# Kernel optimization log

Measured on AMD Instinct MI355X. Metric: run time of the kernel, lower is better.

## Reference

```python
import jax, jax.numpy as jnp
import numpy as np

B, S, D = 2, 2048, 768
H, STRIDE = 12, 8
HD = D // H  # 64


def setup_inputs() -> dict:
    key = jax.random.key(0)
    k0, k1, k2 = jax.random.split(key, 3)
    x = jax.random.normal(k0, (B, S, D), dtype=jnp.float32)
    qkv_w = jax.random.normal(k1, (3 * D, D), dtype=jnp.float32) * 0.02
    qkv_b = jnp.zeros((3 * D,), dtype=jnp.float32)
    out_w = jax.random.normal(k2, (D, D), dtype=jnp.float32) * 0.02
    out_b = jnp.zeros((D,), dtype=jnp.float32)
    return {"x": x, "qkv_w": qkv_w, "qkv_b": qkv_b, "out_w": out_w, "out_b": out_b}


def _stride_mask(S, stride, causal):
    i = jnp.arange(S)[:, None]
    j = jnp.arange(S)[None, :]
    strided = (j % stride == 0)
    if causal:
        strided = strided & (j <= i)
    # diagonal always attended; previous token attended for i > 0
    return strided | (j == i) | (j == i - 1)


def reference(x, qkv_w, qkv_b, out_w, out_b):
    Bx, Sx, Dx = x.shape
    qkv = x @ qkv_w.T + qkv_b                      # [B,S,3D]
    qkv = qkv.reshape(Bx, Sx, 3, H, HD)
    q, k, v = jnp.transpose(qkv, (2, 0, 3, 1, 4))  # each [B,H,S,HD]
    scale = HD ** -0.5
    attn = jnp.einsum('bhid,bhjd->bhij', q, k) * scale  # [B,H,S,S]
    mask = _stride_mask(Sx, STRIDE, True)          # [S,S] bool
    attn = jnp.where(mask[None, None], attn, -jnp.inf)
    a = jax.nn.softmax(attn, axis=-1)
    # every row has at least the diagonal unmasked, so no NaN rows;
    # nan_to_num kept for exact parity with the torch module
    a = jnp.nan_to_num(a, nan=0.0)
    out = jnp.einsum('bhij,bhjd->bhid', a, v)      # [B,H,S,HD]
    out = jnp.transpose(out, (0, 2, 1, 3)).reshape(Bx, Sx, Dx)
    return out @ out_w.T + out_b
```

## Files before the change

kernel.cpp:

```cpp
#include <hip/hip_runtime.h>
#include <hip/hip_bf16.h>
#include <stdint.h>

#define H_   12
#define S_   2048
#define D_   768
#define HD_  64
#define MS_  256

typedef __bf16 bf16_8 __attribute__((ext_vector_type(8)));
typedef float  f32_4  __attribute__((ext_vector_type(4)));

typedef __attribute__((address_space(1))) void* gas_ptr;
typedef __attribute__((address_space(3))) void* las_ptr;

__device__ __forceinline__ void g2l16(const void* g, void* l) {
  __builtin_amdgcn_global_load_lds((gas_ptr)g, (las_ptr)l, 16, 0, 0);
}

__device__ __forceinline__ f32_4 mfma16(bf16_8 a, bf16_8 b, f32_4 c) {
  return __builtin_amdgcn_mfma_f32_16x16x32_bf16(a, b, c, 0, 0, 0);
}

__device__ __forceinline__ bf16_8 ld8(const __hip_bfloat16* p) {
  return *reinterpret_cast<const bf16_8*>(p);
}

__global__ __launch_bounds__(256) void cvt3_f32_bf16(
    const float* __restrict__ a, const float* __restrict__ b,
    const float* __restrict__ c, __hip_bfloat16* __restrict__ out,
    int na4, int nb4) {
  const int t = blockIdx.x * 256 + threadIdx.x;
  float4 f;
  if (t < na4)            f = reinterpret_cast<const float4*>(a)[t];
  else if (t < na4 + nb4) f = reinterpret_cast<const float4*>(b)[t - na4];
  else                    f = reinterpret_cast<const float4*>(c)[t - na4 - nb4];
  union { __hip_bfloat16 h[4]; ushort4 u; } p;
  p.h[0] = __float2bfloat16(f.x);
  p.h[1] = __float2bfloat16(f.y);
  p.h[2] = __float2bfloat16(f.z);
  p.h[3] = __float2bfloat16(f.w);
  reinterpret_cast<ushort4*>(out)[t] = p.u;
}

template <int MODE, int BN>
__global__ __launch_bounds__(256, 4) void gemm_bt(
    const __hip_bfloat16* __restrict__ A, const __hip_bfloat16* __restrict__ B,
    const float* __restrict__ bias,
    __hip_bfloat16* __restrict__ O0, __hip_bfloat16* __restrict__ O1,
    __hip_bfloat16* __restrict__ O2, __hip_bfloat16* __restrict__ O3,
    __hip_bfloat16* __restrict__ O4, float* __restrict__ OF,
    int M, int N, int K) {
  constexpr int NTJ  = BN / 32;
  constexpr int HB   = BN * 32;
  constexpr int DB   = (MODE == 1) ? 2 : 1;
  constexpr int ABUF = 64 * 64;
  constexpr int BBUF = BN * 64;
  __shared__ __bf16 sA[DB * ABUF];
  __shared__ __bf16 sB[DB * BBUF];
  const int tid  = threadIdx.x;
  const int lane = tid & 63;
  const int wv   = tid >> 6;

  const int nwg  = gridDim.x * gridDim.y;
  const int hw   = blockIdx.y * gridDim.x + blockIdx.x;
  const int swz  = (hw & 7) * (nwg >> 3) + (hw >> 3);
  const int bx   = swz % gridDim.x;
  const int by   = swz / gridDim.x;

  const int m0 = by * 64;
  const int n0 = bx * BN;
  const int wr = (wv >> 1) * 32;
  const int wc = (wv & 1) * (BN / 2);

  f32_4 acc[2][NTJ] = {};

  const __hip_bfloat16* aS = A + (size_t)(m0 + (tid >> 2)) * K + ((tid & 3) << 3);
  const __hip_bfloat16* bS = B + (size_t)(n0 + (tid >> 2)) * K + ((tid & 3) << 3);
  const size_t half = (size_t)64 * K;
  __bf16* dA = &sA[tid * 8];
  __bf16* dB = &sB[tid * 8];

  const int fr = lane & 15;
  const int kq = (lane >> 4) << 3;

  auto stage = [&](int k0, int buf) {
    const __hip_bfloat16* a = aS + k0;
    const __hip_bfloat16* b = bS + k0;
    __bf16* da = dA + buf * ABUF;
    __bf16* db = dB + buf * BBUF;
    g2l16(a,      da);
    g2l16(a + 32, da + 2048);
    g2l16(b,      db);
    if constexpr (BN == 128) {
      g2l16(b + half,      db + 2048);
      g2l16(b + 32,        db + 4096);
      g2l16(b + half + 32, db + 4096 + 2048);
    } else {
      g2l16(b + 32, db + 2048);
    }
  };

  auto compute = [&](const __bf16* bA, const __bf16* bB) {
#pragma unroll
    for (int kk = 0; kk < 2; ++kk) {
      bf16_8 af[2], bfm[NTJ];
#pragma unroll
      for (int t = 0; t < 2; ++t)
        af[t] = *reinterpret_cast<const bf16_8*>(
            &bA[kk * 2048 + (wr + t * 16 + fr) * 32 + kq]);
#pragma unroll
      for (int t = 0; t < NTJ; ++t)
        bfm[t] = *reinterpret_cast<const bf16_8*>(
            &bB[kk * HB + (wc + t * 16 + fr) * 32 + kq]);
#pragma unroll
      for (int ti = 0; ti < 2; ++ti)
#pragma unroll
        for (int tj = 0; tj < NTJ; ++tj)
          acc[ti][tj] = mfma16(af[ti], bfm[tj], acc[ti][tj]);
    }
  };

  if constexpr (DB == 1) {
    for (int k0 = 0; k0 < K; k0 += 64) {
      stage(k0, 0);
      __syncthreads();
      compute(sA, sB);
      __syncthreads();
    }
  } else {
    stage(0, 0);
    __syncthreads();
    int cur = 0;
    for (int k0 = 0; k0 < K; k0 += 64) {
      if (k0 + 64 < K) stage(k0 + 64, cur ^ 1);
      compute(&sA[cur * ABUF], &sB[cur * BBUF]);
      __syncthreads();
      cur ^= 1;
    }
  }

  const int crow = (lane >> 4) << 2;
  const int ccol = lane & 15;
#pragma unroll
  for (int ti = 0; ti < 2; ++ti) {
    const int gmb = m0 + wr + ti * 16 + crow;
#pragma unroll
    for (int tj = 0; tj < NTJ; ++tj) {
      const int gn = n0 + wc + tj * 16 + ccol;
      const float bv = bias[gn];
      if (MODE == 0) {
        const int t   = gn / D_;
        const int rem = gn - t * D_;
        const int hh = rem >> 6, dd = rem & 63;
        __hip_bfloat16* dst = (t == 0) ? O0 : (t == 1) ? O1 : O2;
#pragma unroll
        for (int r = 0; r < 4; ++r) {
          const int gm = gmb + r;
          const int bb = gm >> 11, ss = gm & (S_ - 1);
          const __hip_bfloat16 hv = __float2bfloat16(acc[ti][tj][r] + bv);
          dst[(((size_t)(bb * H_ + hh) << 11) + ss) * HD_ + dd] = hv;
          if (r == 0 && (gmb & 7) == 0) {
            if (t == 1)
              O4[(((size_t)(bb * H_ + hh)) * MS_ + (ss >> 3)) * HD_ + dd] = hv;
            else if (t == 2)
              O3[((size_t)(bb * H_ + hh) * HD_ + dd) * MS_ + (ss >> 3)] = hv;
          }
        }
      } else {
#pragma unroll
        for (int r = 0; r < 4; ++r)
          OF[(size_t)(gmb + r) * D_ + gn] = acc[ti][tj][r] + bv;
      }
    }
  }
}

__global__ __launch_bounds__(256) void attn_mfma(
    const __hip_bfloat16* __restrict__ Q, const __hip_bfloat16* __restrict__ Kb,
    const __hip_bfloat16* __restrict__ Ks, const __hip_bfloat16* __restrict__ Vr,
    const __hip_bfloat16* __restrict__ VsT, __hip_bfloat16* __restrict__ ctx) {
  __shared__ __bf16 pt[4][32 * 40];
  __shared__ float ox[3][64][40];
  const int lane = threadIdx.x & 63;
  const int part = threadIdx.x >> 6;
  const int nwg  = gridDim.x;
  const int hw   = blockIdx.x;
  const int task = (hw & 7) * (nwg >> 3) + (hw >> 3);
  const int bh   = task >> 6;
  const int i0   = (task & 63) << 5;
  const int lr   = lane & 15;
  const int quad = lane >> 4;
  const float SC = 0.125f * 1.44269504088896340736f;

  const __hip_bfloat16* Kh  = Kb  + ((size_t)bh << 11) * HD_;
  const __hip_bfloat16* Ksh = Ks  + (size_t)bh * MS_ * HD_;
  const __hip_bfloat16* Vrh = Vr  + ((size_t)bh << 11) * HD_;
  const __hip_bfloat16* Vsh = VsT + (size_t)bh * HD_ * MS_;
  __bf16* ptw = pt[part];

  bf16_8 vfb[4], kb_[2][2];
  int jb = 0;
  if (part >= 2) {
    jb = (part == 3) ? ((i0 >= 8) ? i0 - 8 : 0) : (i0 + 8);
    const __bf16* Vrb = reinterpret_cast<const __bf16*>(Vrh);
#pragma unroll
    for (int ct = 0; ct < 4; ++ct)
#pragma unroll
      for (int e = 0; e < 8; ++e) {
        const int j  = jb + quad * 8 + e;
        const int jr = (j < S_) ? j : (S_ - 1);
        vfb[ct][e] = Vrb[(size_t)jr * HD_ + ct * 16 + lr];
      }
#pragma unroll
    for (int t = 0; t < 2; ++t) {
      const int j  = jb + t * 16 + lr;
      const int jr = (j < S_) ? j : (S_ - 1);
      const __hip_bfloat16* kp = Kh + (size_t)jr * HD_ + quad * 8;
      kb_[t][0] = ld8(kp);
      kb_[t][1] = ld8(kp + 32);
    }
  }

  const __hip_bfloat16* qpA = Q + (((size_t)bh << 11) + i0 + lr) * HD_ + quad * 8;
  const bf16_8 qa0 = ld8(qpA);
  const bf16_8 qa1 = ld8(qpA + 32);
  const __hip_bfloat16* qpB = qpA + (size_t)16 * HD_;
  const bf16_8 qb0 = ld8(qpB);
  const bf16_8 qb1 = ld8(qpB + 32);

  const __bf16 one = (__bf16)1.0f;
  const bf16_8 onesf = {one, one, one, one, one, one, one, one};

  f32_4 LA = {}, LB = {}, oA[4], oB[4];
#pragma unroll
  for (int ct = 0; ct < 4; ++ct) { oA[ct] = f32_4{0.f,0.f,0.f,0.f}; oB[ct] = f32_4{0.f,0.f,0.f,0.f}; }

  const int mmax = (i0 + 31) >> 3;
  const int nstr = (mmax >> 5) + 1;

  auto load_str = [&](int c, bf16_8 (&kf)[2][2], bf16_8 (&vf)[4]) {
    const int mb = c << 5;
#pragma unroll
    for (int t = 0; t < 2; ++t) {
      const __hip_bfloat16* kp = Ksh + (size_t)(mb + t * 16 + lr) * HD_ + quad * 8;
      kf[t][0] = ld8(kp);
      kf[t][1] = ld8(kp + 32);
    }
#pragma unroll
    for (int ct = 0; ct < 4; ++ct)
      vf[ct] = ld8(Vsh + (size_t)(ct * 16 + lr) * MS_ + mb + quad * 8);
  };

  auto softmax_pv = [&](int ro, f32_4& s0, f32_4& s1, const bf16_8 (&vf)[4],
                        f32_4 (&oac)[4], f32_4& La) {
#pragma unroll
    for (int r = 0; r < 4; ++r) {
      const int row = ro + quad * 4 + r;
      ptw[row * 40 + lr]      = (__bf16)__float2bfloat16(s0[r]);
      ptw[row * 40 + 16 + lr] = (__bf16)__float2bfloat16(s1[r]);
    }
    const bf16_8 pf = *reinterpret_cast<const bf16_8*>(&ptw[(ro + lr) * 40 + quad * 8]);
#pragma unroll
    for (int ct = 0; ct < 4; ++ct) oac[ct] = mfma16(pf, vf[ct], oac[ct]);
    La = mfma16(pf, onesf, La);
  };

  bf16_8 kf[2][2], vf[4], kf2[2][2], vf2[4];
  if (part < nstr) load_str(part, kf, vf);
  for (int c = part; c < nstr; c += 4) {
    const bool more = (c + 4 < nstr);
    if (more) load_str(c + 4, kf2, vf2);
    const int mb = c << 5;

    {
      f32_4 s0 = {}, s1 = {};
      s0 = mfma16(qa0, kf[0][0], s0);
      s0 = mfma16(qa1, kf[0][1], s0);
      s1 = mfma16(qa0, kf[1][0], s1);
      s1 = mfma16(qa1, kf[1][1], s1);
#pragma unroll
      for (int r = 0; r < 4; ++r) {
        const int i = i0 + quad * 4 + r;
        const bool v0 = ((mb + lr) << 3) <= i;
        const bool v1 = ((mb + 16 + lr) << 3) <= i;
        s0[r] = v0 ? exp2f(fminf(s0[r] * SC, 63.f)) : 0.f;
        s1[r] = v1 ? exp2f(fminf(s1[r] * SC, 63.f)) : 0.f;
      }
      softmax_pv(0, s0, s1, vf, oA, LA);
    }
    {
      f32_4 s0 = {}, s1 = {};
      s0 = mfma16(qb0, kf[0][0], s0);
      s0 = mfma16(qb1, kf[0][1], s0);
      s1 = mfma16(qb0, kf[1][0], s1);
      s1 = mfma16(qb1, kf[1][1], s1);
#pragma unroll
      for (int r = 0; r < 4; ++r) {
        const int i = i0 + 16 + quad * 4 + r;
        const bool v0 = ((mb + lr) << 3) <= i;
        const bool v1 = ((mb + 16 + lr) << 3) <= i;
        s0[r] = v0 ? exp2f(fminf(s0[r] * SC, 63.f)) : 0.f;
        s1[r] = v1 ? exp2f(fminf(s1[r] * SC, 63.f)) : 0.f;
      }
      softmax_pv(16, s0, s1, vf, oB, LB);
    }

    if (more) {
#pragma unroll
      for (int t = 0; t < 2; ++t) { kf[t][0] = kf2[t][0]; kf[t][1] = kf2[t][1]; }
#pragma unroll
      for (int ct = 0; ct < 4; ++ct) vf[ct] = vf2[ct];
    }
  }

  if (part == 3) {
    f32_4 s0 = {}, s1 = {};
    s0 = mfma16(qa0, kb_[0][0], s0);
    s0 = mfma16(qa1, kb_[0][1], s0);
    s1 = mfma16(qa0, kb_[1][0], s1);
    s1 = mfma16(qa1, kb_[1][1], s1);
#pragma unroll
    for (int r = 0; r < 4; ++r) {
      const int i = i0 + quad * 4 + r;
      const int j0 = jb + lr, j1 = jb + 16 + lr;
      const bool v0 = (j0 == i || j0 == i - 1) && (j0 & 7);
      const bool v1 = (j1 == i || j1 == i - 1) && (j1 & 7);
      s0[r] = v0 ? exp2f(fminf(s0[r] * SC, 63.f)) : 0.f;
      s1[r] = v1 ? exp2f(fminf(s1[r] * SC, 63.f)) : 0.f;
    }
    softmax_pv(0, s0, s1, vfb, oA, LA);
  } else if (part == 2) {
    f32_4 s0 = {}, s1 = {};
    s0 = mfma16(qb0, kb_[0][0], s0);
    s0 = mfma16(qb1, kb_[0][1], s0);
    s1 = mfma16(qb0, kb_[1][0], s1);
    s1 = mfma16(qb1, kb_[1][1], s1);
#pragma unroll
    for (int r = 0; r < 4; ++r) {
      const int i = i0 + 16 + quad * 4 + r;
      const int j0 = jb + lr, j1 = jb + 16 + lr;
      const bool v0 = (j0 == i || j0 == i - 1) && (j0 & 7);
      const bool v1 = (j1 == i || j1 == i - 1) && (j1 & 7);
      s0[r] = v0 ? exp2f(fminf(s0[r] * SC, 63.f)) : 0.f;
      s1[r] = v1 ? exp2f(fminf(s1[r] * SC, 63.f)) : 0.f;
    }
    softmax_pv(16, s0, s1, vfb, oB, LB);
  }

  if (part) {
#pragma unroll
    for (int ct = 0; ct < 4; ++ct)
#pragma unroll
      for (int r = 0; r < 4; ++r) {
        ox[part - 1][lane][ct * 4 + r]      = oA[ct][r];
        ox[part - 1][lane][20 + ct * 4 + r] = oB[ct][r];
      }
#pragma unroll
    for (int r = 0; r < 4; ++r) {
      ox[part - 1][lane][16 + r] = LA[r];
      ox[part - 1][lane][36 + r] = LB[r];
    }
  }
  __syncthreads();

  if (!part) {
#pragma unroll
    for (int p = 0; p < 3; ++p) {
#pragma unroll
      for (int ct = 0; ct < 4; ++ct)
#pragma unroll
        for (int r = 0; r < 4; ++r) {
          oA[ct][r] += ox[p][lane][ct * 4 + r];
          oB[ct][r] += ox[p][lane][20 + ct * 4 + r];
        }
#pragma unroll
      for (int r = 0; r < 4; ++r) {
        LA[r] += ox[p][lane][16 + r];
        LB[r] += ox[p][lane][36 + r];
      }
    }

    const int b = bh / H_;
    const int h = bh - b * H_;
    f32_4 invA, invB;
#pragma unroll
    for (int r = 0; r < 4; ++r) { invA[r] = 1.f / LA[r]; invB[r] = 1.f / LB[r]; }
#pragma unroll
    for (int r = 0; r < 4; ++r) {
      const int iA = i0 + quad * 4 + r;
      __hip_bfloat16* cpA = ctx + ((size_t)(b * S_ + iA)) * D_ + h * HD_ + lr;
#pragma unroll
      for (int ct = 0; ct < 4; ++ct)
        cpA[ct * 16] = __float2bfloat16(oA[ct][r] * invA[r]);
      const int iB = iA + 16;
      __hip_bfloat16* cpB = ctx + ((size_t)(b * S_ + iB)) * D_ + h * HD_ + lr;
#pragma unroll
      for (int ct = 0; ct < 4; ++ct)
        cpB[ct * 16] = __float2bfloat16(oB[ct][r] * invB[r]);
    }
  }
}

extern "C" void kernel_launch(void* const* d_in, const int* in_sizes, int n_in,
                              void* d_out, int out_size, void* d_ws, size_t ws_size,
                              hipStream_t stream) {
  const float* x    = (const float*)d_in[0];
  const float* qkvw = (const float*)d_in[1];
  const float* qkvb = (const float*)d_in[2];
  const float* outw = (const float*)d_in[3];
  const float* outb = (const float*)d_in[4];
  float* out = (float*)d_out;

  const size_t NX  = (size_t)2 * S_ * D_;
  const size_t NW1 = (size_t)3 * D_ * D_;
  const size_t NW2 = (size_t)D_ * D_;
  const size_t NVS = (size_t)2 * H_ * HD_ * MS_;

  __hip_bfloat16* xb  = (__hip_bfloat16*)d_ws;
  __hip_bfloat16* w1b = xb + NX;
  __hip_bfloat16* w2b = w1b + NW1;
  __hip_bfloat16* q   = w2b + NW2;
  __hip_bfloat16* k   = q + NX;
  __hip_bfloat16* vr  = k + NX;
  __hip_bfloat16* vst = vr + NX;
  __hip_bfloat16* ks  = vst + NVS;
  __hip_bfloat16* ctx = ks + NVS;

  const int na4 = (int)(NX / 4), nb4 = (int)(NW1 / 4), nc4 = (int)(NW2 / 4);
  cvt3_f32_bf16<<<dim3((na4 + nb4 + nc4) / 256), 256, 0, stream>>>(
      x, qkvw, outw, xb, na4, nb4);

  gemm_bt<0, 128><<<dim3(2304 / 128, 4096 / 64), 256, 0, stream>>>(
      xb, w1b, qkvb, q, k, vr, vst, ks, nullptr, 4096, 2304, 768);

  attn_mfma<<<dim3(2 * H_ * S_ / 32), 256, 0, stream>>>(
      q, k, ks, vr, vst, ctx);

  gemm_bt<1, 64><<<dim3(768 / 64, 4096 / 64), 256, 0, stream>>>(
      ctx, w2b, outb, nullptr, nullptr, nullptr, nullptr, nullptr,
      out, 4096, 768, 768);
}
```

Measured before the change: 134.7 us.

## Process 64 query rows per attention block to reuse strided K/V loads

Each attention workgroup now handles 64 query rows instead of 32, with four row-groups per wave sharing each loaded strided K/V chunk. The diagonal band work is spread across all four waves (one 16-row group each) instead of two. The grid halves, and the cross-wave reduction runs in two phases through the same shared buffer. The aim is to halve redundant strided K/V loads and launch overhead. In exchange there are more registers per thread, fewer blocks for occupancy, and an extra pair of barriers.

```diff
diff --git a/kernel.cpp b/kernel.cpp
--- a/kernel.cpp
+++ b/kernel.cpp
@@ -180,15 +180,15 @@
     const __hip_bfloat16* __restrict__ Q, const __hip_bfloat16* __restrict__ Kb,
     const __hip_bfloat16* __restrict__ Ks, const __hip_bfloat16* __restrict__ Vr,
     const __hip_bfloat16* __restrict__ VsT, __hip_bfloat16* __restrict__ ctx) {
-  __shared__ __bf16 pt[4][32 * 40];
+  __shared__ __bf16 pt[4][64 * 40];
   __shared__ float ox[3][64][40];
   const int lane = threadIdx.x & 63;
   const int part = threadIdx.x >> 6;
   const int nwg  = gridDim.x;
   const int hw   = blockIdx.x;
   const int task = (hw & 7) * (nwg >> 3) + (hw >> 3);
-  const int bh   = task >> 6;
-  const int i0   = (task & 63) << 5;
+  const int bh   = task >> 5;
+  const int i0   = (task & 31) << 6;
   const int lr   = lane & 15;
   const int quad = lane >> 4;
   const float SC = 0.125f * 1.44269504088896340736f;
@@ -199,10 +199,9 @@
   const __hip_bfloat16* Vsh = VsT + (size_t)bh * HD_ * MS_;
   __bf16* ptw = pt[part];
 
+  const int jb = (part == 0) ? ((i0 >= 8) ? i0 - 8 : 0) : (i0 + 16 * part - 8);
   bf16_8 vfb[4], kb_[2][2];
-  int jb = 0;
-  if (part >= 2) {
-    jb = (part == 3) ? ((i0 >= 8) ? i0 - 8 : 0) : (i0 + 8);
+  {
     const __bf16* Vrb = reinterpret_cast<const __bf16*>(Vrh);
 #pragma unroll
     for (int ct = 0; ct < 4; ++ct)
@@ -222,21 +221,24 @@
     }
   }
 
-  const __hip_bfloat16* qpA = Q + (((size_t)bh << 11) + i0 + lr) * HD_ + quad * 8;
-  const bf16_8 qa0 = ld8(qpA);
-  const bf16_8 qa1 = ld8(qpA + 32);
-  const __hip_bfloat16* qpB = qpA + (size_t)16 * HD_;
-  const bf16_8 qb0 = ld8(qpB);
-  const bf16_8 qb1 = ld8(qpB + 32);
+  const __hip_bfloat16* qp = Q + (((size_t)bh << 11) + i0 + lr) * HD_ + quad * 8;
+  const bf16_8 qA0 = ld8(qp);                       const bf16_8 qA1 = ld8(qp + 32);
+  const bf16_8 qB0 = ld8(qp + (size_t)16 * HD_);    const bf16_8 qB1 = ld8(qp + (size_t)16 * HD_ + 32);
+  const bf16_8 qC0 = ld8(qp + (size_t)32 * HD_);    const bf16_8 qC1 = ld8(qp + (size_t)32 * HD_ + 32);
+  const bf16_8 qD0 = ld8(qp + (size_t)48 * HD_);    const bf16_8 qD1 = ld8(qp + (size_t)48 * HD_ + 32);
 
   const __bf16 one = (__bf16)1.0f;
   const bf16_8 onesf = {one, one, one, one, one, one, one, one};
 
-  f32_4 LA = {}, LB = {}, oA[4], oB[4];
-#pragma unroll
-  for (int ct = 0; ct < 4; ++ct) { oA[ct] = f32_4{0.f,0.f,0.f,0.f}; oB[ct] = f32_4{0.f,0.f,0.f,0.f}; }
-
-  const int mmax = (i0 + 31) >> 3;
+  f32_4 L0 = {}, L1 = {}, L2 = {}, L3 = {};
+  f32_4 o0[4], o1[4], o2[4], o3[4];
+#pragma unroll
+  for (int ct = 0; ct < 4; ++ct) {
+    o0[ct] = f32_4{0.f,0.f,0.f,0.f}; o1[ct] = f32_4{0.f,0.f,0.f,0.f};
+    o2[ct] = f32_4{0.f,0.f,0.f,0.f}; o3[ct] = f32_4{0.f,0.f,0.f,0.f};
+  }
+
+  const int mmax = (i0 + 63) >> 3;
   const int nstr = (mmax >> 5) + 1;
 
   auto load_str = [&](int c, bf16_8 (&kf)[2][2], bf16_8 (&vf)[4]) {
@@ -264,6 +266,25 @@
 #pragma unroll
     for (int ct = 0; ct < 4; ++ct) oac[ct] = mfma16(pf, vf[ct], oac[ct]);
     La = mfma16(pf, onesf, La);
+  };
+
+  auto qkpv = [&](int ro, int mb, bf16_8 q0, bf16_8 q1,
+                  const bf16_8 (&kf)[2][2], const bf16_8 (&vf)[4],
+                  f32_4 (&oac)[4], f32_4& La) {
+    f32_4 s0 = {}, s1 = {};
+    s0 = mfma16(q0, kf[0][0], s0);
+    s0 = mfma16(q1, kf[0][1], s0);
+    s1 = mfma16(q0, kf[1][0], s1);
+    s1 = mfma16(q1, kf[1][1], s1);
+#pragma unroll
+    for (int r = 0; r < 4; ++r) {
+      const int i = i0 + ro + quad * 4 + r;
+      const bool v0 = ((mb + lr) << 3) <= i;
+      const bool v1 = ((mb + 16 + lr) << 3) <= i;
+      s0[r] = v0 ? exp2f(fminf(s0[r] * SC, 63.f)) : 0.f;
+      s1[r] = v1 ? exp2f(fminf(s1[r] * SC, 63.f)) : 0.f;
+    }
+    softmax_pv(ro, s0, s1, vf, oac, La);
   };
 
   bf16_8 kf[2][2], vf[4], kf2[2][2], vf2[4];
@@ -273,38 +294,10 @@
     if (more) load_str(c + 4, kf2, vf2);
     const int mb = c << 5;
 
-    {
-      f32_4 s0 = {}, s1 = {};
-      s0 = mfma16(qa0, kf[0][0], s0);
-      s0 = mfma16(qa1, kf[0][1], s0);
-      s1 = mfma16(qa0, kf[1][0], s1);
-      s1 = mfma16(qa1, kf[1][1], s1);
-#pragma unroll
-      for (int r = 0; r < 4; ++r) {
-        const int i = i0 + quad * 4 + r;
-        const bool v0 = ((mb + lr) << 3) <= i;
-        const bool v1 = ((mb + 16 + lr) << 3) <= i;
-        s0[r] = v0 ? exp2f(fminf(s0[r] * SC, 63.f)) : 0.f;
-        s1[r] = v1 ? exp2f(fminf(s1[r] * SC, 63.f)) : 0.f;
-      }
-      softmax_pv(0, s0, s1, vf, oA, LA);
-    }
-    {
-      f32_4 s0 = {}, s1 = {};
-      s0 = mfma16(qb0, kf[0][0], s0);
-      s0 = mfma16(qb1, kf[0][1], s0);
-      s1 = mfma16(qb0, kf[1][0], s1);
-      s1 = mfma16(qb1, kf[1][1], s1);
-#pragma unroll
-      for (int r = 0; r < 4; ++r) {
-        const int i = i0 + 16 + quad * 4 + r;
-        const bool v0 = ((mb + lr) << 3) <= i;
-        const bool v1 = ((mb + 16 + lr) << 3) <= i;
-        s0[r] = v0 ? exp2f(fminf(s0[r] * SC, 63.f)) : 0.f;
-        s1[r] = v1 ? exp2f(fminf(s1[r] * SC, 63.f)) : 0.f;
-      }
-      softmax_pv(16, s0, s1, vf, oB, LB);
-    }
+    qkpv( 0, mb, qA0, qA1, kf, vf, o0, L0);
+    qkpv(16, mb, qB0, qB1, kf, vf, o1, L1);
+    qkpv(32, mb, qC0, qC1, kf, vf, o2, L2);
+    qkpv(48, mb, qD0, qD1, kf, vf, o3, L3);
 
     if (more) {
 #pragma unroll
@@ -314,56 +307,46 @@
     }
   }
 
-  if (part == 3) {
+  auto band = [&](int ro, bf16_8 q0, bf16_8 q1, f32_4 (&oac)[4], f32_4& La) {
     f32_4 s0 = {}, s1 = {};
-    s0 = mfma16(qa0, kb_[0][0], s0);
-    s0 = mfma16(qa1, kb_[0][1], s0);
-    s1 = mfma16(qa0, kb_[1][0], s1);
-    s1 = mfma16(qa1, kb_[1][1], s1);
-#pragma unroll
-    for (int r = 0; r < 4; ++r) {
-      const int i = i0 + quad * 4 + r;
+    s0 = mfma16(q0, kb_[0][0], s0);
+    s0 = mfma16(q1, kb_[0][1], s0);
+    s1 = mfma16(q0, kb_[1][0], s1);
+    s1 = mfma16(q1, kb_[1][1], s1);
+#pragma unroll
+    for (int r = 0; r < 4; ++r) {
+      const int i = i0 + ro + quad * 4 + r;
       const int j0 = jb + lr, j1 = jb + 16 + lr;
       const bool v0 = (j0 == i || j0 == i - 1) && (j0 & 7);
       const bool v1 = (j1 == i || j1 == i - 1) && (j1 & 7);
       s0[r] = v0 ? exp2f(fminf(s0[r] * SC, 63.f)) : 0.f;
       s1[r] = v1 ? exp2f(fminf(s1[r] * SC, 63.f)) : 0.f;
     }
-    softmax_pv(0, s0, s1, vfb, oA, LA);
-  } else if (part == 2) {
-    f32_4 s0 = {}, s1 = {};
-    s0 = mfma16(qb0, kb_[0][0], s0);
-    s0 = mfma16(qb1, kb_[0][1], s0);
-    s1 = mfma16(qb0, kb_[1][0], s1);
-    s1 = mfma16(qb1, kb_[1][1], s1);
-#pragma unroll
-    for (int r = 0; r < 4; ++r) {
-      const int i = i0 + 16 + quad * 4 + r;
-      const int j0 = jb + lr, j1 = jb + 16 + lr;
-      const bool v0 = (j0 == i || j0 == i - 1) && (j0 & 7);
-      const bool v1 = (j1 == i || j1 == i - 1) && (j1 & 7);
-      s0[r] = v0 ? exp2f(fminf(s0[r] * SC, 63.f)) : 0.f;
-      s1[r] = v1 ? exp2f(fminf(s1[r] * SC, 63.f)) : 0.f;
-    }
-    softmax_pv(16, s0, s1, vfb, oB, LB);
-  }
+    softmax_pv(ro, s0, s1, vfb, oac, La);
+  };
+  if      (part == 0) band( 0, qA0, qA1, o0, L0);
+  else if (part == 1) band(16, qB0, qB1, o1, L1);
+  else if (part == 2) band(32, qC0, qC1, o2, L2);
+  else                band(48, qD0, qD1, o3, L3);
+
+  const int b = bh / H_;
+  const int h = bh - b * H_;
 
   if (part) {
 #pragma unroll
     for (int ct = 0; ct < 4; ++ct)
 #pragma unroll
       for (int r = 0; r < 4; ++r) {
-        ox[part - 1][lane][ct * 4 + r]      = oA[ct][r];
-        ox[part - 1][lane][20 + ct * 4 + r] = oB[ct][r];
-      }
-#pragma unroll
-    for (int r = 0; r < 4; ++r) {
-      ox[part - 1][lane][16 + r] = LA[r];
-      ox[part - 1][lane][36 + r] = LB[r];
+        ox[part - 1][lane][ct * 4 + r]      = o0[ct][r];
+        ox[part - 1][lane][20 + ct * 4 + r] = o1[ct][r];
+      }
+#pragma unroll
+    for (int r = 0; r < 4; ++r) {
+      ox[part - 1][lane][16 + r] = L0[r];
+      ox[part - 1][lane][36 + r] = L1[r];
     }
   }
   __syncthreads();
-
   if (!part) {
 #pragma unroll
     for (int p = 0; p < 3; ++p) {
@@ -371,33 +354,77 @@
       for (int ct = 0; ct < 4; ++ct)
 #pragma unroll
         for (int r = 0; r < 4; ++r) {
-          oA[ct][r] += ox[p][lane][ct * 4 + r];
-          oB[ct][r] += ox[p][lane][20 + ct * 4 + r];
+          o0[ct][r] += ox[p][lane][ct * 4 + r];
+          o1[ct][r] += ox[p][lane][20 + ct * 4 + r];
         }
 #pragma unroll
       for (int r = 0; r < 4; ++r) {
-        LA[r] += ox[p][lane][16 + r];
-        LB[r] += ox[p][lane][36 + r];
-      }
-    }
-
-    const int b = bh / H_;
-    const int h = bh - b * H_;
-    f32_4 invA, invB;
-#pragma unroll
-    for (int r = 0; r < 4; ++r) { invA[r] = 1.f / LA[r]; invB[r] = 1.f / LB[r]; }
+        L0[r] += ox[p][lane][16 + r];
+        L1[r] += ox[p][lane][36 + r];
+      }
+    }
+    f32_4 iv0, iv1;
+#pragma unroll
+    for (int r = 0; r < 4; ++r) { iv0[r] = 1.f / L0[r]; iv1[r] = 1.f / L1[r]; }
 #pragma unroll
     for (int r = 0; r < 4; ++r) {
       const int iA = i0 + quad * 4 + r;
       __hip_bfloat16* cpA = ctx + ((size_t)(b * S_ + iA)) * D_ + h * HD_ + lr;
 #pragma unroll
       for (int ct = 0; ct < 4; ++ct)
-        cpA[ct * 16] = __float2bfloat16(oA[ct][r] * invA[r]);
-      const int iB = iA + 16;
-      __hip_bfloat16* cpB = ctx + ((size_t)(b * S_ + iB)) * D_ + h * HD_ + lr;
-#pragma unroll
-      for (int ct = 0; ct < 4; ++ct)
-        cpB[ct * 16] = __float2bfloat16(oB[ct][r] * invB[r]);
+        cpA[ct * 16] = __float2bfloat16(o0[ct][r] * iv0[r]);
+      __hip_bfloat16* cpB = cpA + (size_t)16 * D_;
+#pragma unroll
+      for (int ct = 0; ct < 4; ++ct)
+        cpB[ct * 16] = __float2bfloat16(o1[ct][r] * iv1[r]);
+    }
+  }
+  __syncthreads();
+  if (part) {
+#pragma unroll
+    for (int ct = 0; ct < 4; ++ct)
+#pragma unroll
+      for (int r = 0; r < 4; ++r) {
+        ox[part - 1][lane][ct * 4 + r]      = o2[ct][r];
+        ox[part - 1][lane][20 + ct * 4 + r] = o3[ct][r];
+      }
+#pragma unroll
+    for (int r = 0; r < 4; ++r) {
+      ox[part - 1][lane][16 + r] = L2[r];
+      ox[part - 1][lane][36 + r] = L3[r];
+    }
+  }
+  __syncthreads();
+  if (!part) {
+#pragma unroll
+    for (int p = 0; p < 3; ++p) {
+#pragma unroll
+      for (int ct = 0; ct < 4; ++ct)
+#pragma unroll
+        for (int r = 0; r < 4; ++r) {
+          o2[ct][r] += ox[p][lane][ct * 4 + r];
+          o3[ct][r] += ox[p][lane][20 + ct * 4 + r];
+        }
+#pragma unroll
+      for (int r = 0; r < 4; ++r) {
+        L2[r] += ox[p][lane][16 + r];
+        L3[r] += ox[p][lane][36 + r];
+      }
+    }
+    f32_4 iv2, iv3;
+#pragma unroll
+    for (int r = 0; r < 4; ++r) { iv2[r] = 1.f / L2[r]; iv3[r] = 1.f / L3[r]; }
+#pragma unroll
+    for (int r = 0; r < 4; ++r) {
+      const int iC = i0 + 32 + quad * 4 + r;
+      __hip_bfloat16* cpC = ctx + ((size_t)(b * S_ + iC)) * D_ + h * HD_ + lr;
+#pragma unroll
+      for (int ct = 0; ct < 4; ++ct)
+        cpC[ct * 16] = __float2bfloat16(o2[ct][r] * iv2[r]);
+      __hip_bfloat16* cpD = cpC + (size_t)16 * D_;
+#pragma unroll
+      for (int ct = 0; ct < 4; ++ct)
+        cpD[ct * 16] = __float2bfloat16(o3[ct][r] * iv3[r]);
     }
   }
 }
@@ -434,7 +461,7 @@
   gemm_bt<0, 128><<<dim3(2304 / 128, 4096 / 64), 256, 0, stream>>>(
       xb, w1b, qkvb, q, k, vr, vst, ks, nullptr, 4096, 2304, 768);
 
-  attn_mfma<<<dim3(2 * H_ * S_ / 32), 256, 0, stream>>>(
+  attn_mfma<<<dim3(2 * H_ * S_ / 64), 256, 0, stream>>>(
       q, k, ks, vr, vst, ctx);
 
   gemm_bt<1, 64><<<dim3(768 / 64, 4096 / 64), 256, 0, stream>>>(
```

Result: slower. 144.9 us (+7.5%).
